# Performance work log

Measured on AMD Instinct MI355X. Metric: run time of the kernel, lower is better.

Reference implementation:

```python
import jax, jax.numpy as jnp
import numpy as np

DIM = 3072
DIM_HEAD = 128
HEADS = 16
KV_DIM = 2048
INNER = DIM_HEAD * HEADS  # 2048


def layernorm(x, g, b, eps=1e-5):
    mu = jnp.mean(x, axis=-1, keepdims=True)
    var = jnp.mean((x - mu) ** 2, axis=-1, keepdims=True)
    return (x - mu) * jax.lax.rsqrt(var + eps) * g + b


def setup_inputs() -> dict:
    key = jax.random.key(0)
    ks = jax.random.split(key, 6)
    b, n1, n2 = 2, 4096, 1024
    x = jax.random.normal(ks[0], (b, n1, KV_DIM), dtype=jnp.float32)
    latents = jax.random.normal(ks[1], (b, n2, DIM), dtype=jnp.float32)
    # Linear weights stored [in, out] (torch stores [out, in]; math is x @ W)
    Wq = jax.random.normal(ks[2], (DIM, INNER), dtype=jnp.float32) * 0.02
    Wkv = jax.random.normal(ks[3], (KV_DIM, 2 * INNER), dtype=jnp.float32) * 0.02
    Wout = jax.random.normal(ks[4], (INNER, DIM), dtype=jnp.float32) * 0.02
    ln1_g = jnp.ones((KV_DIM,), jnp.float32)
    ln1_b = jnp.zeros((KV_DIM,), jnp.float32)
    ln2_g = jnp.ones((DIM,), jnp.float32)
    ln2_b = jnp.zeros((DIM,), jnp.float32)
    return {"x": x, "latents": latents, "ln1_g": ln1_g, "ln1_b": ln1_b,
            "ln2_g": ln2_g, "ln2_b": ln2_b, "Wq": Wq, "Wkv": Wkv, "Wout": Wout}


def reference(x, latents, ln1_g, ln1_b, ln2_g, ln2_b, Wq, Wkv, Wout):
    b, n2, _ = latents.shape
    xn = layernorm(x, ln1_g, ln1_b)          # (b, n1, kv_dim)
    ln = layernorm(latents, ln2_g, ln2_b)    # (b, n2, dim)
    q = ln @ Wq                               # (b, n2, inner)
    kv = xn @ Wkv                             # (b, n1, 2*inner)
    k, v = jnp.split(kv, 2, axis=-1)
    # (b, seq, h*d) -> (b, h, seq, d)
    def heads(t):
        bs, L, _ = t.shape
        return t.reshape(bs, L, HEADS, DIM_HEAD).transpose(0, 2, 1, 3)
    q, k, v = heads(q), heads(k), heads(v)
    scale = 1.0 / np.sqrt(np.sqrt(DIM_HEAD)).astype(np.float32)
    logits = jnp.einsum('bhqd,bhkd->bhqk', q * scale, k * scale)
    w = jax.nn.softmax(logits.astype(jnp.float32), axis=-1).astype(logits.dtype)
    out = jnp.einsum('bhqk,bhkd->bhqd', w, v)  # (b, h, n2, d)
    out = out.transpose(0, 2, 1, 3).reshape(b, n2, INNER)
    return out @ Wout
```

## Files before the change

### kernel.cpp

```cpp
#include <hip/hip_runtime.h>
#include <stdint.h>

typedef unsigned short u16;
typedef unsigned int u32;
typedef __attribute__((ext_vector_type(4))) float f32x4;
typedef __attribute__((ext_vector_type(8))) __bf16 bf16x8;

#define N1T 4096
#define N2T 1024
#define DIMT 3072
#define KVD 2048
#define INN 2048
#define NH 16
#define DH 128

__device__ __forceinline__ u16 f2bf(float f) {
  u32 u = __builtin_bit_cast(u32, f);
  u = (u + 0x7fffu + ((u >> 16) & 1u)) >> 16;
  return (u16)u;
}

__device__ __forceinline__ float exp2_fast(float x) {
  return __builtin_amdgcn_exp2f(x);
}

__device__ __forceinline__ u32 cvtpk(float lo, float hi) {
  u32 r;
  asm volatile("v_cvt_pk_bf16_f32 %0, %1, %2" : "=v"(r) : "v"(lo), "v"(hi));
  return r;
}

typedef __attribute__((address_space(1))) void gvoid_t;
typedef __attribute__((address_space(3))) void lvoid_t;

__device__ __forceinline__ void gload16(const void* g, void* l) {
  __builtin_amdgcn_global_load_lds((gvoid_t*)g, (lvoid_t*)l, 16, 0, 0);
}

template<int NV>
__global__ __launch_bounds__(256) void ln_cast_kernel(
    const float* __restrict__ X, const float* __restrict__ G,
    const float* __restrict__ B, u16* __restrict__ out) {
  const int D = NV * 1024;
  const int t = threadIdx.x;
  const size_t row = blockIdx.x;
  const float4* xr = (const float4*)(X + row * D);
  float4 v[NV];
  float s = 0.f, ss = 0.f;
#pragma unroll
  for (int i = 0; i < NV; ++i) {
    v[i] = xr[i * 256 + t];
    s += v[i].x + v[i].y + v[i].z + v[i].w;
    ss += v[i].x * v[i].x + v[i].y * v[i].y + v[i].z * v[i].z + v[i].w * v[i].w;
  }
#pragma unroll
  for (int off = 32; off; off >>= 1) {
    s += __shfl_xor(s, off);
    ss += __shfl_xor(ss, off);
  }
  __shared__ float red[2][4];
  const int wave = t >> 6, lane = t & 63;
  if (lane == 0) { red[0][wave] = s; red[1][wave] = ss; }
  __syncthreads();
  s = red[0][0] + red[0][1] + red[0][2] + red[0][3];
  ss = red[1][0] + red[1][1] + red[1][2] + red[1][3];
  const float mu = s / D;
  const float rstd = rsqrtf(ss / D - mu * mu + 1e-5f);
  u16* orow = out + row * D;
#pragma unroll
  for (int i = 0; i < NV; ++i) {
    const int idx = (i * 256 + t) * 4;
    float4 g4 = *(const float4*)(G + idx);
    float4 b4 = *(const float4*)(B + idx);
    union { ushort4 v4; u16 h[4]; } pk;
    pk.h[0] = f2bf((v[i].x - mu) * rstd * g4.x + b4.x);
    pk.h[1] = f2bf((v[i].y - mu) * rstd * g4.y + b4.y);
    pk.h[2] = f2bf((v[i].z - mu) * rstd * g4.z + b4.z);
    pk.h[3] = f2bf((v[i].w - mu) * rstd * g4.w + b4.w);
    *(ushort4*)(orow + idx) = pk.v4;
  }
}

__global__ __launch_bounds__(256) void tcast_kernel(
    const float* __restrict__ W, u16* __restrict__ WT, int K, int N) {
  __shared__ __align__(16) u16 tile[64][72];
  const int t = threadIdx.x;
  const int k0 = blockIdx.x * 64, n0 = blockIdx.y * 64;
#pragma unroll
  for (int i = 0; i < 4; ++i) {
    int idx = i * 256 + t;
    int r = idx >> 4, c = (idx & 15) << 2;
    float4 v = *(const float4*)(W + (size_t)(k0 + r) * N + n0 + c);
    union { ushort4 v4; u16 h[4]; } pk;
    pk.h[0] = f2bf(v.x); pk.h[1] = f2bf(v.y);
    pk.h[2] = f2bf(v.z); pk.h[3] = f2bf(v.w);
    *(ushort4*)&tile[r][c] = pk.v4;
  }
  __syncthreads();
#pragma unroll
  for (int j = 0; j < 2; ++j) {
    int cid = j * 256 + t;
    int nr = cid >> 3, kc = (cid & 7) << 3;
    union { uint4 v4; u16 h[8]; } pk;
#pragma unroll
    for (int jj = 0; jj < 8; ++jj) pk.h[jj] = tile[kc + jj][nr];
    *(uint4*)(WT + (size_t)(n0 + nr) * K + k0 + kc) = pk.v4;
  }
}

template<int BF16OUT>
__global__ __launch_bounds__(256) void gemm_bt_kernel(
    const u16* __restrict__ A, size_t Az,
    const u16* __restrict__ Bt, size_t Btz,
    void* __restrict__ Cv, size_t Cz,
    int M, int N, int K, float scale) {
  __shared__ __align__(16) u16 As[128 * 64];
  __shared__ __align__(16) u16 Bs[128 * 64];
  A += (size_t)blockIdx.z * Az;
  Bt += (size_t)blockIdx.z * Btz;
  const int t = threadIdx.x, lane = t & 63, wave = t >> 6;
  const int m0 = blockIdx.x * 128, n0 = blockIdx.y * 128;
  const int wr = (wave >> 1) * 64, wc = (wave & 1) * 64;
  const int fr = lane & 15, fk = (lane >> 4) * 8;
  f32x4 acc[4][4];
#pragma unroll
  for (int i = 0; i < 4; ++i)
#pragma unroll
    for (int j = 0; j < 4; ++j)
#pragma unroll
      for (int r = 0; r < 4; ++r) acc[i][j][r] = 0.f;
  const int srow = t >> 3;
  const int scb = (t & 7) * 16;
  const int nk = K >> 6;
  for (int kt = 0; kt < nk; ++kt) {
    const char* Ab = (const char*)(A + (size_t)kt * 64);
    const char* Bb = (const char*)(Bt + (size_t)kt * 64);
#pragma unroll
    for (int r = 0; r < 4; ++r) {
      int row = srow + r * 32;
      gload16(Ab + (size_t)(m0 + row) * K * 2 + scb, (char*)As + t * 16 + r * 4096);
      gload16(Bb + (size_t)(n0 + row) * K * 2 + scb, (char*)Bs + t * 16 + r * 4096);
    }
    __syncthreads();
#pragma unroll
    for (int kk = 0; kk < 2; ++kk) {
      bf16x8 af[4], bfr[4];
#pragma unroll
      for (int i = 0; i < 4; ++i)
        af[i] = *(const bf16x8*)&As[(wr + i * 16 + fr) * 64 + kk * 32 + fk];
#pragma unroll
      for (int j = 0; j < 4; ++j)
        bfr[j] = *(const bf16x8*)&Bs[(wc + j * 16 + fr) * 64 + kk * 32 + fk];
#pragma unroll
      for (int i = 0; i < 4; ++i)
#pragma unroll
        for (int j = 0; j < 4; ++j)
          acc[i][j] = __builtin_amdgcn_mfma_f32_16x16x32_bf16(af[i], bfr[j], acc[i][j], 0, 0, 0);
    }
    __syncthreads();
  }
  const int cr = (lane >> 4) * 4, cc = lane & 15;
#pragma unroll
  for (int i = 0; i < 4; ++i)
#pragma unroll
    for (int j = 0; j < 4; ++j) {
      const int row = m0 + wr + i * 16 + cr;
      const int col = n0 + wc + j * 16 + cc;
      if (BF16OUT) {
        u16* C = (u16*)Cv + (size_t)blockIdx.z * Cz;
#pragma unroll
        for (int r = 0; r < 4; ++r) C[(size_t)(row + r) * N + col] = f2bf(acc[i][j][r] * scale);
      } else {
        float* C = (float*)Cv + (size_t)blockIdx.z * Cz;
#pragma unroll
        for (int r = 0; r < 4; ++r) C[(size_t)(row + r) * N + col] = acc[i][j][r];
      }
    }
}

__device__ __forceinline__ void stage_region(const u16* __restrict__ G, int ldk,
                                             int rowbase, int colbase,
                                             u16* lds, int t) {
  const int srow = t >> 2, sc = t & 3;
  const int swz = (srow >> 1) & 3;
#pragma unroll
  for (int r = 0; r < 2; ++r) {
    int row = r * 128 + srow;
    gload16(G + (size_t)(rowbase + row) * ldk + colbase + (sc ^ swz) * 8,
            (char*)lds + t * 16 + r * 8192);
  }
}

#define GPHASE(MSUB, KK, STAGE_STMT, RELOAD_B, VM0)                               \
  {                                                                               \
    STAGE_STMT;                                                                   \
    const u16* Aarr = (KK) ? A1s : A0s;                                           \
    _Pragma("unroll")                                                             \
    for (int fi = 0; fi < 4; ++fi) {                                              \
      int rowa = RM + (MSUB) * 64 + fi * 16 + fr;                                 \
      af[fi] = *(const bf16x8*)((const char*)Aarr + rowa * 64 +                   \
                                ((q ^ ((rowa >> 1) & 3)) * 16));                  \
    }                                                                             \
    if (RELOAD_B) {                                                               \
      const u16* Barr = (KK) ? B1s : B0s;                                         \
      _Pragma("unroll")                                                           \
      for (int j = 0; j < 4; ++j) {                                               \
        int rowb = RN + j * 16 + fr;                                              \
        bf[j] = *(const bf16x8*)((const char*)Barr + rowb * 64 +                  \
                                 ((q ^ ((rowb >> 1) & 3)) * 16));                 \
      }                                                                           \
    }                                                                             \
    if (VM0) { asm volatile("s_waitcnt vmcnt(0)" ::: "memory"); }                 \
    else     { asm volatile("s_waitcnt vmcnt(2)" ::: "memory"); }                 \
    __builtin_amdgcn_s_barrier();                                                 \
    asm volatile("s_waitcnt lgkmcnt(0)" ::: "memory");                            \
    __builtin_amdgcn_sched_barrier(0);                                            \
    __builtin_amdgcn_s_setprio(1);                                                \
    _Pragma("unroll")                                                             \
    for (int fi = 0; fi < 4; ++fi)                                                \
      _Pragma("unroll")                                                           \
      for (int j = 0; j < 4; ++j)                                                 \
        acc[(MSUB) * 4 + fi][j] = __builtin_amdgcn_mfma_f32_16x16x32_bf16(        \
            af[fi], bf[j], acc[(MSUB) * 4 + fi][j], 0, 0, 0);                     \
    __builtin_amdgcn_s_setprio(0);                                                \
    __builtin_amdgcn_s_barrier();                                                 \
  }

__device__ __forceinline__ void gemm256_body(
    const u16* __restrict__ A, const u16* __restrict__ Bt, u16* __restrict__ C,
    int N, int K, float scale, int bx, int by,
    u16* A0s, u16* A1s, u16* B0s, u16* B1s, int t) {
  const int lane = t & 63, wave = t >> 6;
  const int m0 = bx * 256, n0 = by * 256;
  const int RM = (wave >> 2) * 128, RN = (wave & 3) * 64;
  const int fr = lane & 15, q = lane >> 4;
  f32x4 acc[8][4];
#pragma unroll
  for (int i = 0; i < 8; ++i)
#pragma unroll
    for (int j = 0; j < 4; ++j)
#pragma unroll
      for (int r = 0; r < 4; ++r) acc[i][j][r] = 0.f;

  stage_region(Bt, K, n0, 0, B0s, t);
  stage_region(A, K, m0, 0, A0s, t);
  stage_region(Bt, K, n0, 32, B1s, t);
  asm volatile("s_waitcnt vmcnt(0)" ::: "memory");
  __builtin_amdgcn_s_barrier();

  const int nk = K >> 6;
#pragma unroll 1
  for (int kt = 0; kt < nk; ++kt) {
    const bool last = (kt == nk - 1);
    bf16x8 af[4], bf[4];
    GPHASE(0, 0, stage_region(A, K, m0, kt * 64 + 32, A1s, t), true, false)
    GPHASE(1, 0, if (!last) stage_region(Bt, K, n0, (kt + 1) * 64, B0s, t), false, last)
    GPHASE(1, 1, if (!last) stage_region(A, K, m0, (kt + 1) * 64, A0s, t), true, last)
    GPHASE(0, 1, if (!last) stage_region(Bt, K, n0, (kt + 1) * 64 + 32, B1s, t), false, last)
  }

  const int cr = (lane >> 4) * 4, cc = lane & 15;
#pragma unroll
  for (int i = 0; i < 8; ++i)
#pragma unroll
    for (int j = 0; j < 4; ++j) {
      const int row = m0 + RM + i * 16 + cr;
      const int col = n0 + RN + j * 16 + cc;
#pragma unroll
      for (int r = 0; r < 4; ++r) C[(size_t)(row + r) * N + col] = f2bf(acc[i][j][r] * scale);
    }
}

__global__ __launch_bounds__(512) void gemm256_dual_kernel(
    const u16* __restrict__ xn, const u16* __restrict__ WkvT,
    u16* __restrict__ kb, u16* __restrict__ vtb, float kscale) {
  __shared__ __align__(16) u16 A0s[256 * 32];
  __shared__ __align__(16) u16 A1s[256 * 32];
  __shared__ __align__(16) u16 B0s[256 * 32];
  __shared__ __align__(16) u16 B1s[256 * 32];
  const int t = threadIdx.x;
  const int bid = blockIdx.x;
  if (bid < 256) {
    gemm256_body(xn, WkvT, kb, 2048, 2048, kscale,
                 bid & 31, bid >> 5, A0s, A1s, B0s, B1s, t);
  } else {
    const int b2 = bid - 256;
    const int z = b2 >> 7, rem = b2 & 127;
    gemm256_body(WkvT + (size_t)2048 * 2048, xn + (size_t)z * 4096 * 2048,
                 vtb + (size_t)z * 2048 * 4096, 4096, 2048, 1.0f,
                 rem & 7, rem >> 3, A0s, A1s, B0s, B1s, t);
  }
}

#define KVB 128
__device__ __forceinline__ int swz4(int row) {
  return ((row & 15) ^ (((row >> 4) & 1) << 2)) << 4;
}

__device__ __forceinline__ void stage_kv(const u16* Kbase, const u16* Vbase,
                                         int kv0, char* ks, char* vs, int t) {
  const int col = (t & 15) * 16;
#pragma unroll
  for (int r = 0; r < 4; ++r) {
    int row = (t >> 4) + r * 32;
    gload16((const char*)(Kbase + (size_t)(kv0 + row) * INN) + (col ^ swz4(row)),
            ks + t * 16 + r * 8192);
  }
#pragma unroll
  for (int r = 0; r < 4; ++r) {
    int row = (t >> 4) + r * 32;
    gload16((const char*)(Vbase + (size_t)row * N1T + kv0) + (col ^ swz4(row)),
            vs + t * 16 + r * 8192);
  }
}

__global__ __launch_bounds__(512, 2) void attn_kernel(
    const u16* __restrict__ Q, const u16* __restrict__ Kb,
    const u16* __restrict__ Vt, float* __restrict__ Opart,
    float* __restrict__ ml) {
  __shared__ __align__(16) u16 Ks[2][KVB * 128];
  __shared__ __align__(16) u16 Vs[2][128 * KVB];
  const int t = threadIdx.x, lane = t & 63, wave = t >> 6;
  const int bid = blockIdx.x;
  const int xcd = bid & 7, idx = bid >> 3;
  const int bh = (xcd << 2) | (idx >> 3);
  const int sub = idx & 7;
  const int qt = sub >> 1, half = sub & 1;
  const int b = bh >> 4, h = bh & 15;
  const int q0 = qt * 256 + wave * 32;
  const int fr = lane & 15, quad = lane >> 4;
  const int fk = quad * 8;
  const int frp = fr + (fr & 12);

  bf16x8 qf0[4], qf1[4];
  {
    const u16* qr0 = Q + (size_t)(b * N2T + q0 + fr) * INN + h * DH;
    const u16* qr1 = Q + (size_t)(b * N2T + q0 + 16 + fr) * INN + h * DH;
#pragma unroll
    for (int c = 0; c < 4; ++c) {
      qf0[c] = *(const bf16x8*)(qr0 + c * 32 + fk);
      qf1[c] = *(const bf16x8*)(qr1 + c * 32 + fk);
    }
  }

  float m_run[2] = {-1e30f, -1e30f}, l_run[2] = {0.f, 0.f};
  f32x4 oT[2][8];
#pragma unroll
  for (int f = 0; f < 2; ++f)
#pragma unroll
    for (int i = 0; i < 8; ++i)
#pragma unroll
      for (int r = 0; r < 4; ++r) oT[f][i][r] = 0.f;

  const u16* Kbase = Kb + (size_t)(b * N1T) * INN + h * DH;
  const u16* Vbase = Vt + ((size_t)b * INN + h * DH) * N1T;
  const int kvb = half * 2048;

  const int NT = 2048 / KVB;
  int cur = 0;
  stage_kv(Kbase, Vbase, kvb, (char*)&Ks[0][0], (char*)&Vs[0][0], t);
  for (int tile = 0; tile < NT; ++tile) {
    if (tile + 1 < NT) {
      stage_kv(Kbase, Vbase, kvb + (tile + 1) * KVB, (char*)&Ks[cur ^ 1][0],
               (char*)&Vs[cur ^ 1][0], t);
      asm volatile("s_waitcnt vmcnt(8)" ::: "memory");
    } else {
      asm volatile("s_waitcnt vmcnt(0)" ::: "memory");
    }
    __builtin_amdgcn_s_barrier();
    __builtin_amdgcn_sched_barrier(0);
    const char* KsC = (const char*)&Ks[cur][0];
    const char* VsC = (const char*)&Vs[cur][0];

    f32x4 sT[2][8];
    __builtin_amdgcn_s_setprio(1);
#pragma unroll
    for (int ni = 0; ni < 8; ++ni) {
#pragma unroll
      for (int r = 0; r < 4; ++r) { sT[0][ni][r] = 0.f; sT[1][ni][r] = 0.f; }
      const int rowa = (ni >> 1) * 32 + (ni & 1) * 4 + frp;
      const int sz = swz4(rowa);
#pragma unroll
      for (int c = 0; c < 4; ++c) {
        bf16x8 kf = *(const bf16x8*)(KsC + rowa * 256 + ((c * 64 + quad * 16) ^ sz));
        sT[0][ni] = __builtin_amdgcn_mfma_f32_16x16x32_bf16(kf, qf0[c], sT[0][ni], 0, 0, 0);
        sT[1][ni] = __builtin_amdgcn_mfma_f32_16x16x32_bf16(kf, qf1[c], sT[1][ni], 0, 0, 0);
      }
    }
    __builtin_amdgcn_s_setprio(0);
    union { u32 w[4]; bf16x8 v; } pa[2][4];
#pragma unroll
    for (int f = 0; f < 2; ++f) {
      float mt = sT[f][0][0];
#pragma unroll
      for (int ni = 0; ni < 8; ++ni)
#pragma unroll
        for (int r = 0; r < 4; ++r) mt = fmaxf(mt, sT[f][ni][r]);
      mt = fmaxf(mt, __shfl_xor(mt, 16));
      mt = fmaxf(mt, __shfl_xor(mt, 32));
      if (!__all(mt <= m_run[f] + 10.f)) {
        float mnew = fmaxf(m_run[f], mt);
        float alpha = exp2_fast(m_run[f] - mnew);
        m_run[f] = mnew;
        l_run[f] *= alpha;
#pragma unroll
        for (int i = 0; i < 8; ++i)
#pragma unroll
          for (int r = 0; r < 4; ++r) oT[f][i][r] *= alpha;
      }
      float lt = 0.f;
#pragma unroll
      for (int ni = 0; ni < 8; ++ni)
#pragma unroll
        for (int r = 0; r < 4; ++r) {
          sT[f][ni][r] = exp2_fast(sT[f][ni][r] - m_run[f]);
          lt += sT[f][ni][r];
        }
      lt += __shfl_xor(lt, 16);
      lt += __shfl_xor(lt, 32);
      l_run[f] += lt;
#pragma unroll
      for (int kk = 0; kk < 4; ++kk) {
        pa[f][kk].w[0] = cvtpk(sT[f][kk * 2][0], sT[f][kk * 2][1]);
        pa[f][kk].w[1] = cvtpk(sT[f][kk * 2][2], sT[f][kk * 2][3]);
        pa[f][kk].w[2] = cvtpk(sT[f][kk * 2 + 1][0], sT[f][kk * 2 + 1][1]);
        pa[f][kk].w[3] = cvtpk(sT[f][kk * 2 + 1][2], sT[f][kk * 2 + 1][3]);
      }
    }
    __builtin_amdgcn_s_setprio(1);
#pragma unroll
    for (int ni2 = 0; ni2 < 8; ++ni2) {
      const int rowv = ni2 * 16 + fr;
      const int sz = swz4(rowv);
#pragma unroll
      for (int kk = 0; kk < 4; ++kk) {
        bf16x8 vf = *(const bf16x8*)(VsC + rowv * 256 + ((kk * 64 + quad * 16) ^ sz));
        oT[0][ni2] = __builtin_amdgcn_mfma_f32_16x16x32_bf16(vf, pa[0][kk].v, oT[0][ni2], 0, 0, 0);
        oT[1][ni2] = __builtin_amdgcn_mfma_f32_16x16x32_bf16(vf, pa[1][kk].v, oT[1][ni2], 0, 0, 0);
      }
    }
    __builtin_amdgcn_s_setprio(0);
    __builtin_amdgcn_sched_barrier(0);
    __builtin_amdgcn_s_barrier();
    cur ^= 1;
  }
#pragma unroll
  for (int f = 0; f < 2; ++f) {
    const size_t row = (size_t)(b * N2T + q0 + f * 16 + fr) * 16 + h;
    float* op = Opart + ((size_t)half * 32768 + row) * 128 + quad * 4;
#pragma unroll
    for (int ni2 = 0; ni2 < 8; ++ni2) {
      float4 v4 = {oT[f][ni2][0], oT[f][ni2][1], oT[f][ni2][2], oT[f][ni2][3]};
      *(float4*)(op + ni2 * 16) = v4;
    }
    if (quad == 0) {
      float2 v2 = {m_run[f], l_run[f]};
      *(float2*)(ml + ((size_t)half * 32768 + row) * 2) = v2;
    }
  }
}

__global__ __launch_bounds__(256) void combine2_kernel(
    const float* __restrict__ Opart, const float* __restrict__ ml,
    u16* __restrict__ ab) {
  const int tid = blockIdx.x * 256 + threadIdx.x;
  const int row = tid >> 5;
  const int c = tid & 31;
  float2 ml1 = *(const float2*)(ml + (size_t)row * 2);
  float2 ml2 = *(const float2*)(ml + ((size_t)32768 + row) * 2);
  float m = fmaxf(ml1.x, ml2.x);
  float w1 = exp2_fast(ml1.x - m), w2 = exp2_fast(ml2.x - m);
  float inv = 1.0f / (w1 * ml1.y + w2 * ml2.y);
  float4 o1 = *(const float4*)(Opart + (size_t)row * 128 + c * 4);
  float4 o2 = *(const float4*)(Opart + ((size_t)32768 + row) * 128 + c * 4);
  union { ushort4 v4; u16 hh[4]; } pk;
  pk.hh[0] = f2bf((w1 * o1.x + w2 * o2.x) * inv);
  pk.hh[1] = f2bf((w1 * o1.y + w2 * o2.y) * inv);
  pk.hh[2] = f2bf((w1 * o1.z + w2 * o2.z) * inv);
  pk.hh[3] = f2bf((w1 * o1.w + w2 * o2.w) * inv);
  *(ushort4*)(ab + (size_t)(row >> 4) * 2048 + (row & 15) * 128 + c * 4) = pk.v4;
}

extern "C" void kernel_launch(void* const* d_in, const int* in_sizes, int n_in,
                              void* d_out, int out_size, void* d_ws, size_t ws_size,
                              hipStream_t stream) {
  const float* x = (const float*)d_in[0];
  const float* latents = (const float*)d_in[1];
  const float* ln1g = (const float*)d_in[2];
  const float* ln1b = (const float*)d_in[3];
  const float* ln2g = (const float*)d_in[4];
  const float* ln2b = (const float*)d_in[5];
  const float* Wq = (const float*)d_in[6];
  const float* Wkv = (const float*)d_in[7];
  const float* Wout = (const float*)d_in[8];

  char* w = (char*)d_ws;
  u16* xn = (u16*)w;   w += (size_t)8192 * 2048 * 2;
  u16* lnb = (u16*)w;  w += (size_t)2048 * 3072 * 2;
  u16* WqT = (u16*)w;  w += (size_t)2048 * 3072 * 2;
  u16* WkvT = (u16*)w; w += (size_t)4096 * 2048 * 2;
  u16* WoT = (u16*)w;  w += (size_t)3072 * 2048 * 2;
  u16* qb = (u16*)w;   w += (size_t)2048 * 2048 * 2;
  u16* kb = (u16*)w;   w += (size_t)8192 * 2048 * 2;
  u16* vtb = (u16*)w;  w += (size_t)2 * 2048 * 4096 * 2;
  u16* ab = (u16*)w;   w += (size_t)2048 * 2048 * 2;
  float* opart = (float*)d_ws;
  float* mlbuf = (float*)((char*)d_ws + 33554432);

  dim3 blk(256);
  tcast_kernel<<<dim3(48, 32), blk, 0, stream>>>(Wq, WqT, 3072, 2048);
  tcast_kernel<<<dim3(32, 64), blk, 0, stream>>>(Wkv, WkvT, 2048, 4096);
  tcast_kernel<<<dim3(32, 48), blk, 0, stream>>>(Wout, WoT, 2048, 3072);
  ln_cast_kernel<2><<<8192, blk, 0, stream>>>(x, ln1g, ln1b, xn);
  ln_cast_kernel<3><<<2048, blk, 0, stream>>>(latents, ln2g, ln2b, lnb);

  const float scale = 0.29730177875068026f;
  const float qscale = scale * 1.4426950408889634f;
  gemm_bt_kernel<1><<<dim3(16, 16, 1), blk, 0, stream>>>(
      lnb, 0, WqT, 0, qb, 0, 2048, 2048, 3072, qscale);
  gemm256_dual_kernel<<<dim3(512), dim3(512), 0, stream>>>(
      xn, WkvT, kb, vtb, scale);
  attn_kernel<<<dim3(256), dim3(512), 0, stream>>>(qb, kb, vtb, opart, mlbuf);
  combine2_kernel<<<dim3(4096), blk, 0, stream>>>(opart, mlbuf, ab);
  gemm_bt_kernel<0><<<dim3(16, 24, 1), blk, 0, stream>>>(
      ab, 0, WoT, 0, d_out, 0, 2048, 3072, 2048, 1.0f);
}
```

Baseline: 386.7 us.

## Split attention KV into quarters with smaller tiles and four-way combine

The attention kernel now splits the key/value sequence into four chunks instead of two. This doubles the grid to 512 blocks, and each block streams 64-key tiles instead of 128. Smaller shared-memory tiles and fewer score registers allow launch bounds of 4 blocks per SM, which is meant to raise occupancy and fill the GPU better. The price is twice as much partial output traffic, written to an enlarged workspace region, and a heavier four-way combine kernel.

Measured after the change: 564.1 us. 45.9% more time.

```diff
diff --git a/kernel.cpp b/kernel.cpp
--- a/kernel.cpp
+++ b/kernel.cpp
@@ -292,29 +292,37 @@
   }
 }
 
-#define KVB 128
-__device__ __forceinline__ int swz4(int row) {
+#define KVB 64
+__device__ __forceinline__ int swzK(int row) {
   return ((row & 15) ^ (((row >> 4) & 1) << 2)) << 4;
+}
+__device__ __forceinline__ int swzV(int row) {
+  return (row & 7) << 4;
 }
 
 __device__ __forceinline__ void stage_kv(const u16* Kbase, const u16* Vbase,
                                          int kv0, char* ks, char* vs, int t) {
-  const int col = (t & 15) * 16;
-#pragma unroll
-  for (int r = 0; r < 4; ++r) {
-    int row = (t >> 4) + r * 32;
-    gload16((const char*)(Kbase + (size_t)(kv0 + row) * INN) + (col ^ swz4(row)),
-            ks + t * 16 + r * 8192);
-  }
-#pragma unroll
-  for (int r = 0; r < 4; ++r) {
-    int row = (t >> 4) + r * 32;
-    gload16((const char*)(Vbase + (size_t)row * N1T + kv0) + (col ^ swz4(row)),
-            vs + t * 16 + r * 8192);
-  }
-}
-
-__global__ __launch_bounds__(512, 2) void attn_kernel(
+  {
+    const int col = (t & 15) * 16;
+#pragma unroll
+    for (int r = 0; r < 2; ++r) {
+      int row = (t >> 4) + r * 32;
+      gload16((const char*)(Kbase + (size_t)(kv0 + row) * INN) + (col ^ swzK(row)),
+              ks + t * 16 + r * 8192);
+    }
+  }
+  {
+    const int col = (t & 7) * 16;
+#pragma unroll
+    for (int r = 0; r < 2; ++r) {
+      int row = (t >> 3) + r * 64;
+      gload16((const char*)(Vbase + (size_t)row * N1T + kv0) + (col ^ swzV(row)),
+              vs + t * 16 + r * 8192);
+    }
+  }
+}
+
+__global__ __launch_bounds__(512, 4) void attn_kernel(
     const u16* __restrict__ Q, const u16* __restrict__ Kb,
     const u16* __restrict__ Vt, float* __restrict__ Opart,
     float* __restrict__ ml) {
@@ -323,9 +331,9 @@
   const int t = threadIdx.x, lane = t & 63, wave = t >> 6;
   const int bid = blockIdx.x;
   const int xcd = bid & 7, idx = bid >> 3;
-  const int bh = (xcd << 2) | (idx >> 3);
-  const int sub = idx & 7;
-  const int qt = sub >> 1, half = sub & 1;
+  const int bh = (xcd << 2) | (idx >> 4);
+  const int sub = idx & 15;
+  const int qt = sub >> 2, quarter = sub & 3;
   const int b = bh >> 4, h = bh & 15;
   const int q0 = qt * 256 + wave * 32;
   const int fr = lane & 15, quad = lane >> 4;
@@ -354,16 +362,16 @@
 
   const u16* Kbase = Kb + (size_t)(b * N1T) * INN + h * DH;
   const u16* Vbase = Vt + ((size_t)b * INN + h * DH) * N1T;
-  const int kvb = half * 2048;
-
-  const int NT = 2048 / KVB;
+  const int kvb = quarter * 1024;
+
+  const int NT = 1024 / KVB;
   int cur = 0;
   stage_kv(Kbase, Vbase, kvb, (char*)&Ks[0][0], (char*)&Vs[0][0], t);
   for (int tile = 0; tile < NT; ++tile) {
     if (tile + 1 < NT) {
       stage_kv(Kbase, Vbase, kvb + (tile + 1) * KVB, (char*)&Ks[cur ^ 1][0],
                (char*)&Vs[cur ^ 1][0], t);
-      asm volatile("s_waitcnt vmcnt(8)" ::: "memory");
+      asm volatile("s_waitcnt vmcnt(4)" ::: "memory");
     } else {
       asm volatile("s_waitcnt vmcnt(0)" ::: "memory");
     }
@@ -372,14 +380,14 @@
     const char* KsC = (const char*)&Ks[cur][0];
     const char* VsC = (const char*)&Vs[cur][0];
 
-    f32x4 sT[2][8];
+    f32x4 sT[2][4];
     __builtin_amdgcn_s_setprio(1);
 #pragma unroll
-    for (int ni = 0; ni < 8; ++ni) {
+    for (int ni = 0; ni < 4; ++ni) {
 #pragma unroll
       for (int r = 0; r < 4; ++r) { sT[0][ni][r] = 0.f; sT[1][ni][r] = 0.f; }
       const int rowa = (ni >> 1) * 32 + (ni & 1) * 4 + frp;
-      const int sz = swz4(rowa);
+      const int sz = swzK(rowa);
 #pragma unroll
       for (int c = 0; c < 4; ++c) {
         bf16x8 kf = *(const bf16x8*)(KsC + rowa * 256 + ((c * 64 + quad * 16) ^ sz));
@@ -388,12 +396,12 @@
       }
     }
     __builtin_amdgcn_s_setprio(0);
-    union { u32 w[4]; bf16x8 v; } pa[2][4];
+    union { u32 w[4]; bf16x8 v; } pa[2][2];
 #pragma unroll
     for (int f = 0; f < 2; ++f) {
       float mt = sT[f][0][0];
 #pragma unroll
-      for (int ni = 0; ni < 8; ++ni)
+      for (int ni = 0; ni < 4; ++ni)
 #pragma unroll
         for (int r = 0; r < 4; ++r) mt = fmaxf(mt, sT[f][ni][r]);
       mt = fmaxf(mt, __shfl_xor(mt, 16));
@@ -410,7 +418,7 @@
       }
       float lt = 0.f;
 #pragma unroll
-      for (int ni = 0; ni < 8; ++ni)
+      for (int ni = 0; ni < 4; ++ni)
 #pragma unroll
         for (int r = 0; r < 4; ++r) {
           sT[f][ni][r] = exp2_fast(sT[f][ni][r] - m_run[f]);
@@ -420,7 +428,7 @@
       lt += __shfl_xor(lt, 32);
       l_run[f] += lt;
 #pragma unroll
-      for (int kk = 0; kk < 4; ++kk) {
+      for (int kk = 0; kk < 2; ++kk) {
         pa[f][kk].w[0] = cvtpk(sT[f][kk * 2][0], sT[f][kk * 2][1]);
         pa[f][kk].w[1] = cvtpk(sT[f][kk * 2][2], sT[f][kk * 2][3]);
         pa[f][kk].w[2] = cvtpk(sT[f][kk * 2 + 1][0], sT[f][kk * 2 + 1][1]);
@@ -431,10 +439,10 @@
 #pragma unroll
     for (int ni2 = 0; ni2 < 8; ++ni2) {
       const int rowv = ni2 * 16 + fr;
-      const int sz = swz4(rowv);
-#pragma unroll
-      for (int kk = 0; kk < 4; ++kk) {
-        bf16x8 vf = *(const bf16x8*)(VsC + rowv * 256 + ((kk * 64 + quad * 16) ^ sz));
+      const int sz = swzV(rowv);
+#pragma unroll
+      for (int kk = 0; kk < 2; ++kk) {
+        bf16x8 vf = *(const bf16x8*)(VsC + rowv * 128 + ((kk * 64 + quad * 16) ^ sz));
         oT[0][ni2] = __builtin_amdgcn_mfma_f32_16x16x32_bf16(vf, pa[0][kk].v, oT[0][ni2], 0, 0, 0);
         oT[1][ni2] = __builtin_amdgcn_mfma_f32_16x16x32_bf16(vf, pa[1][kk].v, oT[1][ni2], 0, 0, 0);
       }
@@ -447,7 +455,7 @@
 #pragma unroll
   for (int f = 0; f < 2; ++f) {
     const size_t row = (size_t)(b * N2T + q0 + f * 16 + fr) * 16 + h;
-    float* op = Opart + ((size_t)half * 32768 + row) * 128 + quad * 4;
+    float* op = Opart + ((size_t)quarter * 32768 + row) * 128 + quad * 4;
 #pragma unroll
     for (int ni2 = 0; ni2 < 8; ++ni2) {
       float4 v4 = {oT[f][ni2][0], oT[f][ni2][1], oT[f][ni2][2], oT[f][ni2][3]};
@@ -455,29 +463,44 @@
     }
     if (quad == 0) {
       float2 v2 = {m_run[f], l_run[f]};
-      *(float2*)(ml + ((size_t)half * 32768 + row) * 2) = v2;
-    }
-  }
-}
-
-__global__ __launch_bounds__(256) void combine2_kernel(
+      *(float2*)(ml + ((size_t)quarter * 32768 + row) * 2) = v2;
+    }
+  }
+}
+
+__global__ __launch_bounds__(256) void combine4_kernel(
     const float* __restrict__ Opart, const float* __restrict__ ml,
     u16* __restrict__ ab) {
   const int tid = blockIdx.x * 256 + threadIdx.x;
   const int row = tid >> 5;
   const int c = tid & 31;
-  float2 ml1 = *(const float2*)(ml + (size_t)row * 2);
-  float2 ml2 = *(const float2*)(ml + ((size_t)32768 + row) * 2);
-  float m = fmaxf(ml1.x, ml2.x);
-  float w1 = exp2_fast(ml1.x - m), w2 = exp2_fast(ml2.x - m);
-  float inv = 1.0f / (w1 * ml1.y + w2 * ml2.y);
-  float4 o1 = *(const float4*)(Opart + (size_t)row * 128 + c * 4);
-  float4 o2 = *(const float4*)(Opart + ((size_t)32768 + row) * 128 + c * 4);
+  float mx[4], ly[4];
+  float m = -1e30f;
+#pragma unroll
+  for (int qd = 0; qd < 4; ++qd) {
+    float2 v = *(const float2*)(ml + ((size_t)qd * 32768 + row) * 2);
+    mx[qd] = v.x; ly[qd] = v.y;
+    m = fmaxf(m, v.x);
+  }
+  float denom = 0.f, wq[4];
+#pragma unroll
+  for (int qd = 0; qd < 4; ++qd) {
+    wq[qd] = exp2_fast(mx[qd] - m);
+    denom += wq[qd] * ly[qd];
+  }
+  const float inv = 1.0f / denom;
+  float ox = 0.f, oy = 0.f, oz = 0.f, ow = 0.f;
+#pragma unroll
+  for (int qd = 0; qd < 4; ++qd) {
+    float4 o = *(const float4*)(Opart + ((size_t)qd * 32768 + row) * 128 + c * 4);
+    ox += wq[qd] * o.x; oy += wq[qd] * o.y;
+    oz += wq[qd] * o.z; ow += wq[qd] * o.w;
+  }
   union { ushort4 v4; u16 hh[4]; } pk;
-  pk.hh[0] = f2bf((w1 * o1.x + w2 * o2.x) * inv);
-  pk.hh[1] = f2bf((w1 * o1.y + w2 * o2.y) * inv);
-  pk.hh[2] = f2bf((w1 * o1.z + w2 * o2.z) * inv);
-  pk.hh[3] = f2bf((w1 * o1.w + w2 * o2.w) * inv);
+  pk.hh[0] = f2bf(ox * inv);
+  pk.hh[1] = f2bf(oy * inv);
+  pk.hh[2] = f2bf(oz * inv);
+  pk.hh[3] = f2bf(ow * inv);
   *(ushort4*)(ab + (size_t)(row >> 4) * 2048 + (row & 15) * 128 + c * 4) = pk.v4;
 }
 
@@ -505,7 +528,7 @@
   u16* vtb = (u16*)w;  w += (size_t)2 * 2048 * 4096 * 2;
   u16* ab = (u16*)w;   w += (size_t)2048 * 2048 * 2;
   float* opart = (float*)d_ws;
-  float* mlbuf = (float*)((char*)d_ws + 33554432);
+  float* mlbuf = (float*)((char*)d_ws + (size_t)67108864 + 4194304);
 
   dim3 blk(256);
   tcast_kernel<<<dim3(48, 32), blk, 0, stream>>>(Wq, WqT, 3072, 2048);
@@ -520,8 +543,8 @@
       lnb, 0, WqT, 0, qb, 0, 2048, 2048, 3072, qscale);
   gemm256_dual_kernel<<<dim3(512), dim3(512), 0, stream>>>(
       xn, WkvT, kb, vtb, scale);
-  attn_kernel<<<dim3(256), dim3(512), 0, stream>>>(qb, kb, vtb, opart, mlbuf);
-  combine2_kernel<<<dim3(4096), blk, 0, stream>>>(opart, mlbuf, ab);
+  attn_kernel<<<dim3(512), dim3(512), 0, stream>>>(qb, kb, vtb, opart, mlbuf);
+  combine4_kernel<<<dim3(4096), blk, 0, stream>>>(opart, mlbuf, ab);
   gemm_bt_kernel<0><<<dim3(16, 24, 1), blk, 0, stream>>>(
       ab, 0, WoT, 0, d_out, 0, 2048, 3072, 2048, 1.0f);
 }
```
